# Performance work log

Measured on AMD Instinct MI355X. Metric: run time of the kernel, lower is better.

## Reference

```python
import jax, jax.numpy as jnp
import numpy as np

EPS = 1e-5
NUM_HEADS = 4
HEAD_DIM = 64
NUM_STEPS = 3


def layernorm(x, g, b):
    mu = jnp.mean(x, axis=-1, keepdims=True)
    var = jnp.mean((x - mu) ** 2, axis=-1, keepdims=True)
    return (x - mu) / jnp.sqrt(var + EPS) * g + b


def entmax15(x):
    # exact alpha=1.5 entmax along last axis (Peters et al. 2019)
    n = x.shape[-1]
    x = x - jnp.max(x, axis=-1, keepdims=True)
    x = x / 2.0
    srt = -jnp.sort(-x, axis=-1)                      # descending
    rho = jnp.arange(1, n + 1, dtype=x.dtype)
    cs = jnp.cumsum(srt, axis=-1)
    cs2 = jnp.cumsum(srt * srt, axis=-1)
    mean = cs / rho
    ss = cs2 - mean * cs                              # k * (mean_sq - mean^2)
    delta = (1.0 - ss) / rho
    d = jnp.clip(delta, 0.0)
    safe = jnp.where(d > 0, d, 1.0)
    tau = mean - jnp.where(d > 0, jnp.sqrt(safe), 0.0)
    support = (tau <= srt).astype(jnp.int32)
    k_star = jnp.sum(support, axis=-1, keepdims=True) - 1
    tau_star = jnp.take_along_axis(tau, k_star, axis=-1)
    p = jnp.clip(x - tau_star, 0.0)
    return p * p


def setup_inputs() -> dict:
    key = jax.random.key(0)
    ks = jax.random.split(key, 8)
    B, S, Dh = 2, 512, 2048
    N, Dm = 8192, 1024
    T = NUM_HEADS * HEAD_DIM  # 256
    hidden = jax.random.normal(ks[0], (B, S, Dh), dtype=jnp.float32)
    memory = jax.random.normal(ks[1], (N, Dm), dtype=jnp.float32)
    Wq = jax.random.normal(ks[2], (Dh, T), dtype=jnp.float32) * 0.02
    Wk = jax.random.normal(ks[3], (Dm, T), dtype=jnp.float32) * 0.02
    Wv = jax.random.normal(ks[4], (Dm, T), dtype=jnp.float32) * 0.02
    Wo = jax.random.normal(ks[5], (T, Dh), dtype=jnp.float32) * 0.02
    log_beta = jnp.full((NUM_HEADS,), float(np.log(1.0 / np.sqrt(HEAD_DIM))), dtype=jnp.float32)
    g_s = jnp.ones((Dh,), jnp.float32)
    b_s = jnp.zeros((Dh,), jnp.float32)
    g_m = jnp.ones((Dm,), jnp.float32)
    b_m = jnp.zeros((Dm,), jnp.float32)
    return {"hidden": hidden, "memory": memory, "Wq": Wq, "Wk": Wk, "Wv": Wv,
            "Wo": Wo, "log_beta": log_beta, "g_s": g_s, "b_s": b_s,
            "g_m": g_m, "b_m": b_m}


def reference(hidden, memory, Wq, Wk, Wv, Wo, log_beta, g_s, b_s, g_m, b_m):
    B, S, _ = hidden.shape
    N = memory.shape[0]
    H, D = NUM_HEADS, HEAD_DIM
    Q = layernorm(hidden, g_s, b_s) @ Wq                         # [B,S,H*D]
    mem_n = layernorm(memory, g_m, b_m)
    K = (mem_n @ Wk).reshape(N, H, D).transpose(1, 0, 2)         # [H,N,D]
    V = (mem_n @ Wv).reshape(N, H, D).transpose(1, 0, 2)         # [H,N,D]
    xi = Q.reshape(B, S, H, D).transpose(0, 2, 1, 3)             # [B,H,S,D]
    beta = jnp.exp(log_beta)[None, :, None, None]                # [1,H,1,1]
    for _ in range(NUM_STEPS):
        scores = jnp.einsum('bhsd,hnd->bhsn', xi, K) * beta      # [B,H,S,N]
        w = entmax15(scores)
        xi = jnp.einsum('bhsn,hnd->bhsd', w, V)
    converged = xi.transpose(0, 2, 1, 3).reshape(B, S, H * D)
    output = converged @ Wo                                      # [B,S,hidden_dim]
    return output, converged
```

## Files before the change

kernel.cpp:

```cpp
#include <hip/hip_runtime.h>
#include <math.h>

typedef _Float16 f16;
typedef f16 f16x8 __attribute__((ext_vector_type(8)));
typedef float f32x4 __attribute__((ext_vector_type(4)));

#define QSCALE 16384.0f
#define QINV 6.103515625e-5f
#define QOFF 2.5f

__device__ __forceinline__ float wred_add(float v) {
#pragma unroll
  for (int off = 32; off >= 1; off >>= 1) v += __shfl_xor(v, off, 64);
  return v;
}
__device__ __forceinline__ float wred_max(float v) {
#pragma unroll
  for (int off = 32; off >= 1; off >>= 1) v = fmaxf(v, __shfl_xor(v, off, 64));
  return v;
}

__global__ __launch_bounds__(256) void ln_stats_all_kernel(
    const float* __restrict__ hidden, const float* __restrict__ memory,
    float* __restrict__ mu_h, float* __restrict__ rs_h,
    float* __restrict__ mu_m, float* __restrict__ rs_m) {
  int b = blockIdx.x, tid = threadIdx.x;
  const float* X;
  float* mu;
  float* rs;
  int cols, row;
  if (b < 1024) { X = hidden; cols = 2048; mu = mu_h; rs = rs_h; row = b; }
  else { X = memory; cols = 1024; mu = mu_m; rs = rs_m; row = b - 1024; }
  const float4* xr = (const float4*)(X + (size_t)row * cols);
  int nv = cols >> 10;
  float s = 0.f, s2 = 0.f;
  for (int v = 0; v < nv; ++v) {
    float4 x4 = xr[tid + (v << 8)];
    s += x4.x + x4.y + x4.z + x4.w;
    s2 += x4.x * x4.x + x4.y * x4.y + x4.z * x4.z + x4.w * x4.w;
  }
  s = wred_add(s);
  s2 = wred_add(s2);
  __shared__ float rb[8];
  int wid = tid >> 6, lane = tid & 63;
  if (lane == 0) { rb[wid] = s; rb[4 + wid] = s2; }
  __syncthreads();
  if (tid == 0) {
    float S = rb[0] + rb[1] + rb[2] + rb[3];
    float S2 = rb[4] + rb[5] + rb[6] + rb[7];
    float m = S / (float)cols;
    float var = S2 / (float)cols - m * m;
    mu[row] = m;
    rs[row] = 1.f / sqrtf(var + 1e-5f);
  }
}

__global__ __launch_bounds__(256) void split_a_all_kernel(
    const float* __restrict__ hidden, const float* __restrict__ memory,
    const float* __restrict__ mu_h, const float* __restrict__ rs_h,
    const float* __restrict__ mu_m, const float* __restrict__ rs_m,
    f16x8* __restrict__ Ahh, f16x8* __restrict__ Ahl,
    f16x8* __restrict__ Amh, f16x8* __restrict__ Aml) {
  int b = blockIdx.x;
  const float* X;
  const float* mu;
  const float* rs;
  f16x8 *Ah, *Al;
  int M, Kd, b0;
  if (b < 1024) {
    X = hidden; mu = mu_h; rs = rs_h; Ah = Ahh; Al = Ahl;
    M = 1024; Kd = 2048; b0 = 0;
  } else {
    X = memory; mu = mu_m; rs = rs_m; Ah = Amh; Al = Aml;
    M = 8192; Kd = 1024; b0 = 1024;
  }
  int blk = (b - b0) * 4 + (threadIdx.x >> 6);
  int l = threadIdx.x & 63;
  int nmt = M >> 4;
  int kc = blk / nmt, mt = blk - kc * nmt;
  int m = mt * 16 + (l & 15);
  int k = kc * 32 + ((l >> 4) << 3);
  const float* src = X + (size_t)m * Kd + k;
  float mm = mu[m];
  float rr = rs[m];
  f16x8 hi, lo;
#pragma unroll
  for (int j = 0; j < 8; ++j) {
    float v = (src[j] - mm) * rr;
    f16 hv = (f16)v;
    hi[j] = hv;
    lo[j] = (f16)((v - (float)hv) * 512.f);
  }
  size_t o = ((size_t)blk << 6) + l;
  Ah[o] = hi;
  Al[o] = lo;
}

__global__ __launch_bounds__(256) void split_a_kernel(
    const float* __restrict__ X, const float* __restrict__ mu,
    const float* __restrict__ rs, f16x8* __restrict__ Ah,
    f16x8* __restrict__ Al, int M, int Kd, int lay) {
  int blk = blockIdx.x * 4 + (threadIdx.x >> 6);
  int l = threadIdx.x & 63;
  int nmt = M >> 4;
  int kc = blk / nmt, mt = blk - kc * nmt;
  int m = mt * 16 + (l & 15);
  int k = kc * 32 + ((l >> 4) << 3);
  const float* src;
  if (lay == 0) {
    src = X + (size_t)m * Kd + k;
  } else {
    int b = m >> 9, s = m & 511, hh = k >> 6, d = k & 63;
    src = X + ((((size_t)b * 4 + hh) * 512 + s) << 6) + d;
  }
  float mm = mu ? mu[m] : 0.f;
  float rr = rs ? rs[m] : 1.f;
  f16x8 hi, lo;
#pragma unroll
  for (int j = 0; j < 8; ++j) {
    float v = (src[j] - mm) * rr;
    f16 hv = (f16)v;
    hi[j] = hv;
    lo[j] = (f16)((v - (float)hv) * 512.f);
  }
  size_t o = ((size_t)blk << 6) + l;
  Ah[o] = hi;
  Al[o] = lo;
}

__global__ __launch_bounds__(256) void split_w_all_kernel(
    const float* __restrict__ Wq, const float* __restrict__ Wk,
    const float* __restrict__ Wv, const float* __restrict__ Wo,
    const float* __restrict__ g_s, const float* __restrict__ g_m,
    f16x8* __restrict__ Bqh, f16x8* __restrict__ Bql,
    f16x8* __restrict__ Bkh, f16x8* __restrict__ Bkl,
    f16x8* __restrict__ Bvh, f16x8* __restrict__ Bvl,
    f16x8* __restrict__ Boh, f16x8* __restrict__ Bol) {
  int b = blockIdx.x;
  const float* W;
  const float* g;
  f16x8 *Bh, *Bl;
  int N, base;
  if (b < 256) { W = Wq; g = g_s; Bh = Bqh; Bl = Bql; N = 256; base = 0; }
  else if (b < 384) { W = Wk; g = g_m; Bh = Bkh; Bl = Bkl; N = 256; base = 256; }
  else if (b < 512) { W = Wv; g = g_m; Bh = Bvh; Bl = Bvl; N = 256; base = 384; }
  else { W = Wo; g = nullptr; Bh = Boh; Bl = Bol; N = 2048; base = 512; }
  int blk = (b - base) * 4 + (threadIdx.x >> 6);
  int l = threadIdx.x & 63;
  int nnt = N >> 4;
  int kc = blk / nnt, nt = blk - kc * nnt;
  int n = nt * 16 + (l & 15);
  int k0 = kc * 32 + ((l >> 4) << 3);
  f16x8 hi, lo;
#pragma unroll
  for (int j = 0; j < 8; ++j) {
    float v = W[(size_t)(k0 + j) * N + n];
    if (g) v *= g[k0 + j];
    f16 hv = (f16)v;
    hi[j] = hv;
    lo[j] = (f16)((v - (float)hv) * 512.f);
  }
  size_t o = ((size_t)blk << 6) + l;
  Bh[o] = hi;
  Bl[o] = lo;
}

__global__ __launch_bounds__(256) void wcol3_kernel(
    const float* __restrict__ Wq, const float* __restrict__ bq,
    const float* __restrict__ Wk, const float* __restrict__ bk,
    const float* __restrict__ Wv, const float* __restrict__ bv,
    float* __restrict__ vbq, float* __restrict__ vbk,
    float* __restrict__ vbv) {
  int which = blockIdx.z;
  const float* W = which == 0 ? Wq : (which == 1 ? Wk : Wv);
  const float* b = which == 0 ? bq : (which == 1 ? bk : bv);
  float* vb = which == 0 ? vbq : (which == 1 ? vbk : vbv);
  int Kd = which == 0 ? 2048 : 1024;
  int t = threadIdx.x;
  int kpb = Kd >> 4;
  int k0 = blockIdx.y * kpb;
  float s = 0.f;
  for (int k = k0; k < k0 + kpb; ++k) s = fmaf(b[k], W[(size_t)k * 256 + t], s);
  atomicAdd(&vb[t], s);
}

__global__ __launch_bounds__(256) void gemm_mfma_kernel(
    const f16x8* __restrict__ Ah, const f16x8* __restrict__ Al,
    const f16x8* __restrict__ Bh, const f16x8* __restrict__ Bl,
    const float* __restrict__ vb, float* __restrict__ outf,
    f16x8* __restrict__ o16a, f16x8* __restrict__ o16b, int M, int N, int nk,
    int out_mode) {
  __shared__ __align__(16) float Ts[64][68];
  const int tid = threadIdx.x;
  const int w = tid >> 6, l = tid & 63;
  const int ql = l & 15, g = l >> 4;
  const int bn = blockIdx.x, bm = blockIdx.y;
  const size_t astr = ((size_t)(M >> 4)) << 6;
  const size_t bstr = ((size_t)(N >> 4)) << 6;
  const f16x8* aph = Ah + (((size_t)(bm * 4 + w)) << 6) + l;
  const f16x8* apl = Al + (((size_t)(bm * 4 + w)) << 6) + l;
  const f16x8* bph = Bh + (((size_t)(bn * 4)) << 6) + l;
  const f16x8* bpl = Bl + (((size_t)(bn * 4)) << 6) + l;

  f32x4 cm[4], cx[4];
#pragma unroll
  for (int nf = 0; nf < 4; ++nf) {
    cm[nf] = (f32x4){0.f, 0.f, 0.f, 0.f};
    cx[nf] = (f32x4){0.f, 0.f, 0.f, 0.f};
  }

  f16x8 a0h = aph[0], a0l = apl[0];
  f16x8 b0h[4], b0l[4];
#pragma unroll
  for (int nf = 0; nf < 4; ++nf) {
    b0h[nf] = bph[nf << 6];
    b0l[nf] = bpl[nf << 6];
  }

  for (int kc = 0; kc < nk - 1; ++kc) {
    const size_t ao = (size_t)(kc + 1) * astr;
    const size_t bo = (size_t)(kc + 1) * bstr;
    f16x8 a1h = aph[ao], a1l = apl[ao];
    f16x8 b1h[4], b1l[4];
#pragma unroll
    for (int nf = 0; nf < 4; ++nf) {
      b1h[nf] = bph[bo + (nf << 6)];
      b1l[nf] = bpl[bo + (nf << 6)];
    }
#pragma unroll
    for (int nf = 0; nf < 4; ++nf) {
      cm[nf] = __builtin_amdgcn_mfma_f32_16x16x32_f16(a0h, b0h[nf], cm[nf], 0, 0, 0);
      cx[nf] = __builtin_amdgcn_mfma_f32_16x16x32_f16(a0h, b0l[nf], cx[nf], 0, 0, 0);
      cx[nf] = __builtin_amdgcn_mfma_f32_16x16x32_f16(a0l, b0h[nf], cx[nf], 0, 0, 0);
    }
    a0h = a1h;
    a0l = a1l;
#pragma unroll
    for (int nf = 0; nf < 4; ++nf) {
      b0h[nf] = b1h[nf];
      b0l[nf] = b1l[nf];
    }
  }
#pragma unroll
  for (int nf = 0; nf < 4; ++nf) {
    cm[nf] = __builtin_amdgcn_mfma_f32_16x16x32_f16(a0h, b0h[nf], cm[nf], 0, 0, 0);
    cx[nf] = __builtin_amdgcn_mfma_f32_16x16x32_f16(a0h, b0l[nf], cx[nf], 0, 0, 0);
    cx[nf] = __builtin_amdgcn_mfma_f32_16x16x32_f16(a0l, b0h[nf], cx[nf], 0, 0, 0);
  }

  float vbc[4] = {0.f, 0.f, 0.f, 0.f};
  if (vb) {
#pragma unroll
    for (int nf = 0; nf < 4; ++nf) vbc[nf] = vb[bn * 64 + nf * 16 + ql];
  }

  if (out_mode == 0) {
#pragma unroll
    for (int nf = 0; nf < 4; ++nf)
#pragma unroll
      for (int r = 0; r < 4; ++r) {
        float val = fmaf(cx[nf][r], 0.001953125f, cm[nf][r]) + vbc[nf];
        int m = bm * 64 + w * 16 + (g << 2) + r;
        int n = bn * 64 + nf * 16 + ql;
        int b = m >> 9, s = m & 511, hh = n >> 6, d = n & 63;
        outf[((((size_t)b * 4 + hh) * 512 + s) << 6) + d] = val;
      }
  } else if (out_mode == 3) {
#pragma unroll
    for (int nf = 0; nf < 4; ++nf)
#pragma unroll
      for (int r = 0; r < 4; ++r) {
        float val = fmaf(cx[nf][r], 0.001953125f, cm[nf][r]) + vbc[nf];
        int m = bm * 64 + w * 16 + (g << 2) + r;
        int n = bn * 64 + nf * 16 + ql;
        outf[(size_t)m * N + n] = val;
      }
  } else {
#pragma unroll
    for (int nf = 0; nf < 4; ++nf)
#pragma unroll
      for (int r = 0; r < 4; ++r)
        Ts[w * 16 + (g << 2) + r][nf * 16 + ql] =
            fmaf(cx[nf][r], 0.001953125f, cm[nf][r]) + vbc[nf];
    __syncthreads();
    if (out_mode == 4) {
#pragma unroll
      for (int i = 0; i < 2; ++i) {
        int slot = tid + (i << 8);
        int blk = slot >> 6, l2 = slot & 63;
        int ktl = blk >> 1, dc = blk & 1;
        int key = (ktl << 4) + (l2 & 15);
        int db = (dc << 5) + ((l2 >> 4) << 3);
        f16x8 hi, lo;
#pragma unroll
        for (int j = 0; j < 8; ++j) {
          float v = Ts[key][db + j];
          f16 hv = (f16)v;
          hi[j] = hv;
          lo[j] = (f16)((v - (float)hv) * 512.f);
        }
        size_t o = (((size_t)(bn * 512 + bm * 4 + ktl) * 2 + dc) << 6) + l2;
        o16a[o] = hi;
        o16b[o] = lo;
      }
    } else {
#pragma unroll
      for (int i = 0; i < 2; ++i) {
        int slot = tid + (i << 8);
        int blk = slot >> 6, l2 = slot & 63;
        int dt = blk >> 1, kcl = blk & 1;
        int keyb = (kcl << 5) + ((l2 >> 4) << 3);
        int d = (dt << 4) + (l2 & 15);
        f16x8 v8;
#pragma unroll
        for (int j = 0; j < 8; ++j) v8[j] = (f16)Ts[keyb + j][d];
        size_t o = (((size_t)(bn * 4 + dt) * 256 + bm * 2 + kcl) << 6) + l2;
        o16a[o] = v8;
      }
    }
  }
}

__global__ __launch_bounds__(1024) void hop_score_kernel(
    const float* __restrict__ xi_in, const f16x8* __restrict__ Khi,
    const f16x8* __restrict__ Klo, const float* __restrict__ log_beta,
    unsigned short* __restrict__ Y) {
  __shared__ float xiq[16][64];
  __shared__ float mxb[16][16];
  __shared__ float mxs[16];
  const int tid = threadIdx.x;
  const int w = tid >> 6, l = tid & 63;
  const int ql = l & 15, g = l >> 4;
  const int bh = blockIdx.x & 7, qtile = blockIdx.x >> 3;
  const int h = bh & 3;
  const size_t base_io = ((size_t)bh * 512 + qtile * 16) * 64;

  float beta = expf(log_beta[h]);
  xiq[tid >> 6][tid & 63] = xi_in[base_io + tid] * beta;
  __syncthreads();

  f16x8 xh0, xh1, xl0, xl1;
#pragma unroll
  for (int j = 0; j < 8; ++j) {
    float x0 = xiq[ql][(g << 3) + j];
    float x1 = xiq[ql][32 + (g << 3) + j];
    f16 h0 = (f16)x0, h1 = (f16)x1;
    xh0[j] = h0; xl0[j] = (f16)((x0 - (float)h0) * 512.f);
    xh1[j] = h1; xl1[j] = (f16)((x1 - (float)h1) * 512.f);
  }

  const f16x8* kb = Khi + (size_t)h * 65536 + l;
  const f16x8* kl = Klo + (size_t)h * 65536 + l;
  const int kt0 = w * 32;

  float mymax;
  {
    f32x4 c = {0.f, 0.f, 0.f, 0.f};
    c = __builtin_amdgcn_mfma_f32_16x16x32_f16(kb[(size_t)kt0 * 128], xh0, c, 0, 0, 0);
    c = __builtin_amdgcn_mfma_f32_16x16x32_f16(kb[(size_t)kt0 * 128 + 64], xh1, c, 0, 0, 0);
    mymax = fmaxf(fmaxf(c[0], c[1]), fmaxf(c[2], c[3]));
  }
  mymax = fmaxf(mymax, __shfl_xor(mymax, 16, 64));
  mymax = fmaxf(mymax, __shfl_xor(mymax, 32, 64));
  if (l < 16) mxb[w][ql] = mymax;
  __syncthreads();
  if (tid < 16) {
    float m = mxb[0][tid];
#pragma unroll
    for (int ww = 1; ww < 16; ++ww) m = fmaxf(m, mxb[ww][tid]);
    mxs[tid] = m;
  }
  __syncthreads();
  const float mh = mxs[ql] * 0.5f;
  const float qc = QOFF * QSCALE + 0.5f - mh * QSCALE;

  const size_t Ybase = (size_t)(bh * 32 + qtile) * 131072;
  for (int kt = kt0; kt < kt0 + 32; ++kt) {
    f16x8 a0 = kb[(size_t)kt * 128], a1 = kb[(size_t)kt * 128 + 64];
    f16x8 b0 = kl[(size_t)kt * 128], b1 = kl[(size_t)kt * 128 + 64];
    f32x4 cm = {0.f, 0.f, 0.f, 0.f}, cx = {0.f, 0.f, 0.f, 0.f};
    cm = __builtin_amdgcn_mfma_f32_16x16x32_f16(a0, xh0, cm, 0, 0, 0);
    cm = __builtin_amdgcn_mfma_f32_16x16x32_f16(a1, xh1, cm, 0, 0, 0);
    cx = __builtin_amdgcn_mfma_f32_16x16x32_f16(b0, xh0, cx, 0, 0, 0);
    cx = __builtin_amdgcn_mfma_f32_16x16x32_f16(a0, xl0, cx, 0, 0, 0);
    cx = __builtin_amdgcn_mfma_f32_16x16x32_f16(b1, xh1, cx, 0, 0, 0);
    cx = __builtin_amdgcn_mfma_f32_16x16x32_f16(a1, xl1, cx, 0, 0, 0);
    ushort4 uv;
    unsigned short* up = (unsigned short*)&uv;
#pragma unroll
    for (int r = 0; r < 4; ++r) {
      float s = fmaf(cx[r], 0.001953125f, cm[r]);
      float uq = fmaf(s, 8192.0f, qc);
      uq = fminf(fmaxf(uq, 0.f), 65535.f);
      up[r] = (unsigned short)(int)uq;
    }
    *(ushort4*)&Y[Ybase + (size_t)(kt >> 1) * 512 + ql * 32 + (kt & 1) * 16 +
                  (g << 2)] = uv;
  }
}

__global__ __launch_bounds__(256) void hop_tau_kernel(
    const unsigned short* __restrict__ Y, float* __restrict__ tau) {
  const int row = blockIdx.x;
  const int bh = row >> 9, qi = row & 511;
  const int qtile = qi >> 4, ql = qi & 15;
  const size_t yb = (size_t)(bh * 32 + qtile) * 131072 + ql * 32;
  const int t = threadIdx.x;
  const uint4* p = (const uint4*)(Y + yb + (size_t)t * 512);
  float y[32];
#pragma unroll
  for (int v = 0; v < 4; ++v) {
    uint4 u = p[v];
    unsigned a[4] = {u.x, u.y, u.z, u.w};
#pragma unroll
    for (int e = 0; e < 4; ++e) {
      y[v * 8 + e * 2] = fmaf((float)(a[e] & 0xffffu), QINV, -QOFF);
      y[v * 8 + e * 2 + 1] = fmaf((float)(a[e] >> 16), QINV, -QOFF);
    }
  }
  __shared__ float redm[4];
  __shared__ float rb[5][4];
  __shared__ float rb3[3][4][3];
  const int wi = t >> 6, lane = t & 63;

  {
    float m = y[0];
#pragma unroll
    for (int i = 1; i < 32; ++i) m = fmaxf(m, y[i]);
    m = wred_max(m);
    if (lane == 0) redm[wi] = m;
  }
  __syncthreads();
  const float ymax =
      fmaxf(fmaxf(redm[0], redm[1]), fmaxf(redm[2], redm[3]));

  float lo = ymax - 1.001f, hi = ymax;
#pragma unroll 1
  for (int it = 0; it < 5; ++it) {
    float tv = 0.5f * (lo + hi);
    float f = 0.f;
#pragma unroll
    for (int i = 0; i < 32; ++i) {
      float d = fmaxf(y[i] - tv, 0.f);
      f = fmaf(d, d, f);
    }
    f = wred_add(f);
    if (lane == 0) rb[it][wi] = f;
    __syncthreads();
    float tot = rb[it][0] + rb[it][1] + rb[it][2] + rb[it][3];
    if (tot >= 1.f) lo = tv; else hi = tv;
  }

  float tc = lo;
#pragma unroll 1
  for (int it = 0; it < 3; ++it) {
    float kk = 0.f, s1 = 0.f, s2 = 0.f;
#pragma unroll
    for (int i = 0; i < 32; ++i) {
      if (y[i] > tc) { kk += 1.f; s1 += y[i]; s2 = fmaf(y[i], y[i], s2); }
    }
    kk = wred_add(kk);
    s1 = wred_add(s1);
    s2 = wred_add(s2);
    if (lane == 0) { rb3[it][wi][0] = kk; rb3[it][wi][1] = s1; rb3[it][wi][2] = s2; }
    __syncthreads();
    float K = rb3[it][0][0] + rb3[it][1][0] + rb3[it][2][0] + rb3[it][3][0];
    float S1 = rb3[it][0][1] + rb3[it][1][1] + rb3[it][2][1] + rb3[it][3][1];
    float S2 = rb3[it][0][2] + rb3[it][1][2] + rb3[it][2][2] + rb3[it][3][2];
    if (K >= 0.5f) {
      float mean = S1 / K;
      float ss = fmaf(-mean, S1, S2);
      float delta = (1.f - ss) / K;
      tc = delta > 0.f ? mean - sqrtf(delta) : mean;
    }
  }
  if (t == 0) tau[row] = tc;
}

__global__ __launch_bounds__(1024) void hop_pv_kernel(
    const unsigned short* __restrict__ Y, const f16x8* __restrict__ Vp,
    const float* __restrict__ tau, float* __restrict__ xi_out) {
  __shared__ float outp[16][16][64];
  __shared__ float taus[16];
  const int tid = threadIdx.x;
  const int w = tid >> 6, l = tid & 63;
  const int ql = l & 15, g = l >> 4;
  const int bh = blockIdx.x & 7, qtile = blockIdx.x >> 3;
  const int h = bh & 3;
  const size_t base_io = ((size_t)bh * 512 + qtile * 16) * 64;

  if (tid < 16) taus[tid] = tau[bh * 512 + qtile * 16 + tid];
  __syncthreads();
  const float t1 = taus[ql];
  const size_t Ybase = (size_t)(bh * 32 + qtile) * 131072;
  const f16x8* vb = Vp + (size_t)h * 65536 + l;

  f32x4 m2[4];
#pragma unroll
  for (int dt = 0; dt < 4; ++dt) m2[dt] = (f32x4){0.f, 0.f, 0.f, 0.f};

  for (int kc = 0; kc < 16; ++kc) {
    const int chunk = w * 16 + kc;
    uint4 uv = *(const uint4*)(Y + Ybase + (size_t)chunk * 512 + ql * 32 +
                               (g << 3));
    unsigned a[4] = {uv.x, uv.y, uv.z, uv.w};
    f16x8 a2;
#pragma unroll
    for (int e = 0; e < 4; ++e) {
      float y0 = fmaf((float)(a[e] & 0xffffu), QINV, -QOFF);
      float y1 = fmaf((float)(a[e] >> 16), QINV, -QOFF);
      float p0 = fmaxf(y0 - t1, 0.f);
      float p1 = fmaxf(y1 - t1, 0.f);
      a2[e * 2] = (f16)(p0 * p0);
      a2[e * 2 + 1] = (f16)(p1 * p1);
    }
#pragma unroll
    for (int dt = 0; dt < 4; ++dt) {
      f16x8 vf = vb[(((size_t)dt * 256 + chunk) << 6)];
      m2[dt] = __builtin_amdgcn_mfma_f32_16x16x32_f16(a2, vf, m2[dt], 0, 0, 0);
    }
  }
#pragma unroll
  for (int dt = 0; dt < 4; ++dt)
#pragma unroll
    for (int r = 0; r < 4; ++r)
      outp[w][(g << 2) + r][dt * 16 + ql] = m2[dt][r];
  __syncthreads();
  {
    float s = 0.f;
#pragma unroll
    for (int ww = 0; ww < 16; ++ww) s += outp[ww][tid >> 6][tid & 63];
    xi_out[base_io + tid] = s;
  }
}

__global__ __launch_bounds__(256) void conv_copy_kernel(
    const float* __restrict__ xi, float* __restrict__ out) {
  int o4 = blockIdx.x * 256 + threadIdx.x;
  int o = o4 << 2;
  int dd = o & 63, hq = (o >> 6) & 3, sq = (o >> 8) & 511, bq = o >> 17;
  float4 v =
      *(const float4*)&xi[((((size_t)bq << 2) + hq) * 512 + sq) * 64 + dd];
  *(float4*)&out[o] = v;
}

extern "C" void kernel_launch(void* const* d_in, const int* in_sizes, int n_in,
                              void* d_out, int out_size, void* d_ws,
                              size_t ws_size, hipStream_t stream) {
  (void)in_sizes; (void)n_in; (void)out_size; (void)ws_size;
  const float* hidden = (const float*)d_in[0];
  const float* memory = (const float*)d_in[1];
  const float* Wq = (const float*)d_in[2];
  const float* Wk = (const float*)d_in[3];
  const float* Wv = (const float*)d_in[4];
  const float* Wo = (const float*)d_in[5];
  const float* log_beta = (const float*)d_in[6];
  const float* g_s = (const float*)d_in[7];
  const float* b_s = (const float*)d_in[8];
  const float* g_m = (const float*)d_in[9];
  const float* b_m = (const float*)d_in[10];
  float* out = (float*)d_out;

  float* ws = (float*)d_ws;
  float* mu_h = ws;
  float* rs_h = ws + 1024;
  float* mu_m = ws + 2048;
  float* rs_m = ws + 10240;
  float* xiA = ws + 18432;
  float* xiB = ws + 280576;
  float* vb_q = ws + 542720;
  float* vb_k = ws + 542976;
  float* vb_v = ws + 543232;
  float* tau = ws + 543488;
  f16x8* Khi = (f16x8*)(ws + 548864);
  f16x8* Klo = Khi + 262144;
  f16x8* Vp = Klo + 262144;
  f16x8* Bqh = Vp + 262144;
  f16x8* Bql = Bqh + 65536;
  f16x8* Bkh = Bql + 65536;
  f16x8* Bkl = Bkh + 32768;
  f16x8* Bvh = Bkl + 32768;
  f16x8* Bvl = Bvh + 32768;
  f16x8* Boh = Bvl + 32768;
  f16x8* Bol = Boh + 65536;
  unsigned short* Y = (unsigned short*)(Bol + 65536);
  f16x8* Amh = (f16x8*)Y;
  f16x8* Aml = Amh + 1048576;
  f16x8* Ahh = Aml + 1048576;
  f16x8* Ahl = Ahh + 262144;
  f16x8* Axh = Ahl + 262144;
  f16x8* Axl = Axh + 32768;

  ln_stats_all_kernel<<<9216, 256, 0, stream>>>(hidden, memory, mu_h, rs_h,
                                                mu_m, rs_m);
  hipMemsetAsync(vb_q, 0, 3 * 256 * sizeof(float), stream);

  split_a_all_kernel<<<5120, 256, 0, stream>>>(hidden, memory, mu_h, rs_h,
                                               mu_m, rs_m, Ahh, Ahl, Amh, Aml);
  split_w_all_kernel<<<768, 256, 0, stream>>>(Wq, Wk, Wv, Wo, g_s, g_m, Bqh,
                                              Bql, Bkh, Bkl, Bvh, Bvl, Boh,
                                              Bol);
  wcol3_kernel<<<dim3(1, 16, 3), 256, 0, stream>>>(Wq, b_s, Wk, b_m, Wv, b_m,
                                                   vb_q, vb_k, vb_v);

  gemm_mfma_kernel<<<dim3(4, 16), 256, 0, stream>>>(
      Ahh, Ahl, Bqh, Bql, vb_q, xiA, nullptr, nullptr, 1024, 256, 64, 0);
  gemm_mfma_kernel<<<dim3(4, 128), 256, 0, stream>>>(
      Amh, Aml, Bkh, Bkl, vb_k, nullptr, Khi, Klo, 8192, 256, 32, 4);
  gemm_mfma_kernel<<<dim3(4, 128), 256, 0, stream>>>(
      Amh, Aml, Bvh, Bvl, vb_v, nullptr, Vp, nullptr, 8192, 256, 32, 5);

  float* xin = xiA;
  float* xout = xiB;
  for (int step = 0; step < 3; ++step) {
    hop_score_kernel<<<256, 1024, 0, stream>>>(xin, Khi, Klo, log_beta, Y);
    hop_tau_kernel<<<4096, 256, 0, stream>>>(Y, tau);
    hop_pv_kernel<<<256, 1024, 0, stream>>>(Y, Vp, tau, xout);
    float* t = xin; xin = xout; xout = t;
  }

  split_a_kernel<<<128, 256, 0, stream>>>(xin, nullptr, nullptr, Axh, Axl,
                                          1024, 256, 1);
  gemm_mfma_kernel<<<dim3(32, 16), 256, 0, stream>>>(
      Axh, Axl, Boh, Bol, nullptr, out, nullptr, nullptr, 1024, 2048, 8, 3);
  conv_copy_kernel<<<256, 256, 0, stream>>>(xin, out + 2097152);
}
```

Measured before the change: 420.1 us.

## Fuse score, tau solve and PV into a single hop step kernel

Merges the three per-step kernels (score, entmax threshold solve, PV) into one block-level kernel. Each wave computes tau for one query row by rereading the quantized scores from global memory (mostly L2) on every bisection and Newton pass, instead of holding them in registers. The max is now found on the raw uint16 codes. This removes two launches per step and the tau round trip through global memory. In exchange, the threshold phase runs on only 256 blocks of 16 waves each, far fewer than the 4096 blocks used before, and it repeats global loads on every iteration.

```diff
diff --git a/kernel.cpp b/kernel.cpp
--- a/kernel.cpp
+++ b/kernel.cpp
@@ -321,19 +321,23 @@
   }
 }
 
-__global__ __launch_bounds__(1024) void hop_score_kernel(
+__global__ __launch_bounds__(1024) void hop_step_kernel(
     const float* __restrict__ xi_in, const f16x8* __restrict__ Khi,
-    const f16x8* __restrict__ Klo, const float* __restrict__ log_beta,
-    unsigned short* __restrict__ Y) {
+    const f16x8* __restrict__ Klo, const f16x8* __restrict__ Vp,
+    const float* __restrict__ log_beta, unsigned short* __restrict__ Y,
+    float* __restrict__ xi_out) {
   __shared__ float xiq[16][64];
   __shared__ float mxb[16][16];
   __shared__ float mxs[16];
+  __shared__ float taus[16];
+  __shared__ float outp[16][16][64];
   const int tid = threadIdx.x;
   const int w = tid >> 6, l = tid & 63;
   const int ql = l & 15, g = l >> 4;
   const int bh = blockIdx.x & 7, qtile = blockIdx.x >> 3;
   const int h = bh & 3;
   const size_t base_io = ((size_t)bh * 512 + qtile * 16) * 64;
+  const size_t Ybase = (size_t)(bh * 32 + qtile) * 131072;
 
   float beta = expf(log_beta[h]);
   xiq[tid >> 6][tid & 63] = xi_in[base_io + tid] * beta;
@@ -374,7 +378,6 @@
   const float mh = mxs[ql] * 0.5f;
   const float qc = QOFF * QSCALE + 0.5f - mh * QSCALE;
 
-  const size_t Ybase = (size_t)(bh * 32 + qtile) * 131072;
   for (int kt = kt0; kt < kt0 + 32; ++kt) {
     f16x8 a0 = kb[(size_t)kt * 128], a1 = kb[(size_t)kt * 128 + 64];
     f16x8 b0 = kl[(size_t)kt * 128], b1 = kl[(size_t)kt * 128 + 64];
@@ -397,104 +400,98 @@
     *(ushort4*)&Y[Ybase + (size_t)(kt >> 1) * 512 + ql * 32 + (kt & 1) * 16 +
                   (g << 2)] = uv;
   }
-}
-
-__global__ __launch_bounds__(256) void hop_tau_kernel(
-    const unsigned short* __restrict__ Y, float* __restrict__ tau) {
-  const int row = blockIdx.x;
-  const int bh = row >> 9, qi = row & 511;
-  const int qtile = qi >> 4, ql = qi & 15;
-  const size_t yb = (size_t)(bh * 32 + qtile) * 131072 + ql * 32;
-  const int t = threadIdx.x;
-  const uint4* p = (const uint4*)(Y + yb + (size_t)t * 512);
-  float y[32];
-#pragma unroll
-  for (int v = 0; v < 4; ++v) {
-    uint4 u = p[v];
-    unsigned a[4] = {u.x, u.y, u.z, u.w};
-#pragma unroll
-    for (int e = 0; e < 4; ++e) {
-      y[v * 8 + e * 2] = fmaf((float)(a[e] & 0xffffu), QINV, -QOFF);
-      y[v * 8 + e * 2 + 1] = fmaf((float)(a[e] >> 16), QINV, -QOFF);
-    }
-  }
-  __shared__ float redm[4];
-  __shared__ float rb[5][4];
-  __shared__ float rb3[3][4][3];
-  const int wi = t >> 6, lane = t & 63;
+  __syncthreads();
 
   {
-    float m = y[0];
-#pragma unroll
-    for (int i = 1; i < 32; ++i) m = fmaxf(m, y[i]);
-    m = wred_max(m);
-    if (lane == 0) redm[wi] = m;
+    const unsigned short* rowp = Y + Ybase + (size_t)w * 32;
+    unsigned um = 0;
+#pragma unroll
+    for (int j = 0; j < 4; ++j) {
+      const uint4* pp = (const uint4*)(rowp + (size_t)(4 * l + j) * 512);
+#pragma unroll
+      for (int v = 0; v < 4; ++v) {
+        uint4 u = pp[v];
+        unsigned ww0 = u.x, ww1 = u.y, ww2 = u.z, ww3 = u.w;
+        unsigned m01 = (ww0 & 0xffffu) > (ww0 >> 16) ? (ww0 & 0xffffu) : (ww0 >> 16);
+        unsigned m23 = (ww1 & 0xffffu) > (ww1 >> 16) ? (ww1 & 0xffffu) : (ww1 >> 16);
+        unsigned m45 = (ww2 & 0xffffu) > (ww2 >> 16) ? (ww2 & 0xffffu) : (ww2 >> 16);
+        unsigned m67 = (ww3 & 0xffffu) > (ww3 >> 16) ? (ww3 & 0xffffu) : (ww3 >> 16);
+        unsigned ma = m01 > m23 ? m01 : m23;
+        unsigned mb = m45 > m67 ? m45 : m67;
+        unsigned mc = ma > mb ? ma : mb;
+        if (mc > um) um = mc;
+      }
+    }
+#pragma unroll
+    for (int off = 32; off >= 1; off >>= 1) {
+      unsigned o = (unsigned)__shfl_xor((int)um, off, 64);
+      if (o > um) um = o;
+    }
+    const float ymax = fmaf((float)um, QINV, -QOFF);
+
+    float lo = ymax - 1.001f, hi = ymax;
+#pragma unroll 1
+    for (int it = 0; it < 5; ++it) {
+      float tv = 0.5f * (lo + hi);
+      float f = 0.f;
+#pragma unroll
+      for (int j = 0; j < 4; ++j) {
+        const uint4* pp = (const uint4*)(rowp + (size_t)(4 * l + j) * 512);
+#pragma unroll
+        for (int v = 0; v < 4; ++v) {
+          uint4 u = pp[v];
+          unsigned a[4] = {u.x, u.y, u.z, u.w};
+#pragma unroll
+          for (int e = 0; e < 4; ++e) {
+            float y0 = fmaf((float)(a[e] & 0xffffu), QINV, -QOFF);
+            float y1 = fmaf((float)(a[e] >> 16), QINV, -QOFF);
+            float d0 = fmaxf(y0 - tv, 0.f);
+            float d1 = fmaxf(y1 - tv, 0.f);
+            f = fmaf(d0, d0, f);
+            f = fmaf(d1, d1, f);
+          }
+        }
+      }
+      f = wred_add(f);
+      if (f >= 1.f) lo = tv; else hi = tv;
+    }
+
+    float tc = lo;
+#pragma unroll 1
+    for (int it = 0; it < 3; ++it) {
+      float kk = 0.f, s1 = 0.f, s2 = 0.f;
+#pragma unroll
+      for (int j = 0; j < 4; ++j) {
+        const uint4* pp = (const uint4*)(rowp + (size_t)(4 * l + j) * 512);
+#pragma unroll
+        for (int v = 0; v < 4; ++v) {
+          uint4 u = pp[v];
+          unsigned a[4] = {u.x, u.y, u.z, u.w};
+#pragma unroll
+          for (int e = 0; e < 4; ++e) {
+            float y0 = fmaf((float)(a[e] & 0xffffu), QINV, -QOFF);
+            float y1 = fmaf((float)(a[e] >> 16), QINV, -QOFF);
+            if (y0 > tc) { kk += 1.f; s1 += y0; s2 = fmaf(y0, y0, s2); }
+            if (y1 > tc) { kk += 1.f; s1 += y1; s2 = fmaf(y1, y1, s2); }
+          }
+        }
+      }
+      kk = wred_add(kk);
+      s1 = wred_add(s1);
+      s2 = wred_add(s2);
+      if (kk >= 0.5f) {
+        float mean = s1 / kk;
+        float ss = fmaf(-mean, s1, s2);
+        float delta = (1.f - ss) / kk;
+        tc = delta > 0.f ? mean - sqrtf(delta) : mean;
+      }
+    }
+    if (l == 0) taus[w] = tc;
   }
   __syncthreads();
-  const float ymax =
-      fmaxf(fmaxf(redm[0], redm[1]), fmaxf(redm[2], redm[3]));
-
-  float lo = ymax - 1.001f, hi = ymax;
-#pragma unroll 1
-  for (int it = 0; it < 5; ++it) {
-    float tv = 0.5f * (lo + hi);
-    float f = 0.f;
-#pragma unroll
-    for (int i = 0; i < 32; ++i) {
-      float d = fmaxf(y[i] - tv, 0.f);
-      f = fmaf(d, d, f);
-    }
-    f = wred_add(f);
-    if (lane == 0) rb[it][wi] = f;
-    __syncthreads();
-    float tot = rb[it][0] + rb[it][1] + rb[it][2] + rb[it][3];
-    if (tot >= 1.f) lo = tv; else hi = tv;
-  }
-
-  float tc = lo;
-#pragma unroll 1
-  for (int it = 0; it < 3; ++it) {
-    float kk = 0.f, s1 = 0.f, s2 = 0.f;
-#pragma unroll
-    for (int i = 0; i < 32; ++i) {
-      if (y[i] > tc) { kk += 1.f; s1 += y[i]; s2 = fmaf(y[i], y[i], s2); }
-    }
-    kk = wred_add(kk);
-    s1 = wred_add(s1);
-    s2 = wred_add(s2);
-    if (lane == 0) { rb3[it][wi][0] = kk; rb3[it][wi][1] = s1; rb3[it][wi][2] = s2; }
-    __syncthreads();
-    float K = rb3[it][0][0] + rb3[it][1][0] + rb3[it][2][0] + rb3[it][3][0];
-    float S1 = rb3[it][0][1] + rb3[it][1][1] + rb3[it][2][1] + rb3[it][3][1];
-    float S2 = rb3[it][0][2] + rb3[it][1][2] + rb3[it][2][2] + rb3[it][3][2];
-    if (K >= 0.5f) {
-      float mean = S1 / K;
-      float ss = fmaf(-mean, S1, S2);
-      float delta = (1.f - ss) / K;
-      tc = delta > 0.f ? mean - sqrtf(delta) : mean;
-    }
-  }
-  if (t == 0) tau[row] = tc;
-}
-
-__global__ __launch_bounds__(1024) void hop_pv_kernel(
-    const unsigned short* __restrict__ Y, const f16x8* __restrict__ Vp,
-    const float* __restrict__ tau, float* __restrict__ xi_out) {
-  __shared__ float outp[16][16][64];
-  __shared__ float taus[16];
-  const int tid = threadIdx.x;
-  const int w = tid >> 6, l = tid & 63;
-  const int ql = l & 15, g = l >> 4;
-  const int bh = blockIdx.x & 7, qtile = blockIdx.x >> 3;
-  const int h = bh & 3;
-  const size_t base_io = ((size_t)bh * 512 + qtile * 16) * 64;
-
-  if (tid < 16) taus[tid] = tau[bh * 512 + qtile * 16 + tid];
-  __syncthreads();
+
   const float t1 = taus[ql];
-  const size_t Ybase = (size_t)(bh * 32 + qtile) * 131072;
   const f16x8* vb = Vp + (size_t)h * 65536 + l;
-
   f32x4 m2[4];
 #pragma unroll
   for (int dt = 0; dt < 4; ++dt) m2[dt] = (f32x4){0.f, 0.f, 0.f, 0.f};
@@ -572,6 +569,7 @@
   float* vb_k = ws + 542976;
   float* vb_v = ws + 543232;
   float* tau = ws + 543488;
+  (void)tau;
   f16x8* Khi = (f16x8*)(ws + 548864);
   f16x8* Klo = Khi + 262144;
   f16x8* Vp = Klo + 262144;
@@ -613,9 +611,8 @@
   float* xin = xiA;
   float* xout = xiB;
   for (int step = 0; step < 3; ++step) {
-    hop_score_kernel<<<256, 1024, 0, stream>>>(xin, Khi, Klo, log_beta, Y);
-    hop_tau_kernel<<<4096, 256, 0, stream>>>(Y, tau);
-    hop_pv_kernel<<<256, 1024, 0, stream>>>(Y, Vp, tau, xout);
+    hop_step_kernel<<<256, 1024, 0, stream>>>(xin, Khi, Klo, Vp, log_beta, Y,
+                                              xout);
     float* t = xin; xin = xout; xout = t;
   }
 
```

New measurement: 521.5 us. +24.2%, slower.
